# Optimization experiments

Hardware: AMD Instinct MI355X
Metric: run time of the kernel (lower is better)

## Reference

```python
import jax, jax.numpy as jnp
import numpy as np

B, S, T = 32, 512, 2048
D_TXT, D_MEL = 256, 80


def conv1d(x, w, b, pad):
    # x: (B, C_in, L), w: (C_out, C_in, K)
    y = jax.lax.conv_general_dilated(x, w, window_strides=(1,), padding=[(pad, pad)],
                                     dimension_numbers=('NCH', 'OIH', 'NCH'))
    return y + b[None, :, None]


def text_encoder(x, tw1, tb1, tw2, tb2):
    h = jax.nn.relu(conv1d(x, tw1, tb1, 1))
    return conv1d(h, tw2, tb2, 0)


def mel_encoder(x, mw1, mb1, mw2, mb2, mw3, mb3):
    h = jax.nn.leaky_relu(conv1d(x, mw1, mb1, 1), 0.01)
    h = jax.nn.leaky_relu(conv1d(h, mw2, mb2, 1), 0.01)
    return conv1d(h, mw3, mb3, 0)


def cdist(a, b):
    # a: (B,S,D), b: (B,T,D) -> (B,S,T) euclidean (torch.cdist p=2)
    d2 = (jnp.sum(a * a, -1)[:, :, None] + jnp.sum(b * b, -1)[:, None, :]
          - 2.0 * jnp.einsum('bsd,btd->bst', a, b))
    return jnp.sqrt(jnp.maximum(d2, 1e-12))


def maximum_path(value, mask):
    # Glow-TTS monotonic alignment search. value, mask: (B,S,T) float.
    b, s, t = value.shape
    neg_inf = jnp.float32(-jnp.inf)
    val = (value * mask).transpose(2, 0, 1)  # (T,B,S)
    x_range = jnp.arange(s)

    def fwd_step(v, jc):
        j, col = jc
        v0 = jnp.concatenate([jnp.full((b, 1), neg_inf, v.dtype), v[:, :-1]], axis=1)
        keep = v >= v0  # True: best predecessor is same text index
        v_max = jnp.where(keep, v, v0)
        v_new = jnp.where(x_range[None, :] <= j, v_max + col, neg_inf)
        return v_new, keep

    _, dirs = jax.lax.scan(fwd_step, jnp.zeros((b, s), value.dtype), (jnp.arange(t), val))
    direction = jnp.where(mask.astype(bool), dirs.transpose(1, 2, 0), True).astype(jnp.int32)

    index0 = jnp.sum(mask[:, :, 0], axis=1).astype(jnp.int32) - 1

    def bwd_step(index, dcol):
        row = (jnp.arange(s)[None, :] == index[:, None]).astype(value.dtype)
        d = jnp.take_along_axis(dcol, index[:, None], axis=1)[:, 0]
        return index + d - 1, row

    dcols_rev = jnp.flip(direction, axis=2).transpose(2, 0, 1)  # (T,B,S)
    _, rows = jax.lax.scan(bwd_step, index0, dcols_rev)
    path = jnp.flip(rows, axis=0).transpose(1, 2, 0)  # (B,S,T)
    return path * mask


def setup_inputs() -> dict:
    key = jax.random.key(0)
    ks = jax.random.split(key, 16)
    text = jax.random.normal(ks[0], (B, S, D_TXT), jnp.float32)
    mel = jax.random.normal(ks[1], (B, T, D_MEL), jnp.float32)
    src_len = jax.random.randint(ks[2], (B,), S // 2, S + 1).astype(jnp.int32)
    mel_len = jax.random.randint(ks[3], (B,), T // 2, T + 1).astype(jnp.int32)
    src_mask = jnp.arange(S)[None, :] >= src_len[:, None]   # True = pad
    mel_mask = jnp.arange(T)[None, :] >= mel_len[:, None]
    attn_mask = jnp.zeros((B, S, T), bool)  # unused in forward
    sc = 0.05
    params = dict(
        tw1=jax.random.normal(ks[4], (512, 256, 3)) * sc, tb1=jnp.zeros((512,)),
        tw2=jax.random.normal(ks[5], (80, 512, 1)) * sc, tb2=jnp.zeros((80,)),
        mw1=jax.random.normal(ks[6], (160, 80, 3)) * sc, mb1=jnp.zeros((160,)),
        mw2=jax.random.normal(ks[7], (80, 160, 3)) * sc, mb2=jnp.zeros((80,)),
        mw3=jax.random.normal(ks[8], (80, 80, 1)) * sc, mb3=jnp.zeros((80,)),
    )
    return dict(text=text, mel=mel, src_len=src_len, mel_len=mel_len,
                src_mask=src_mask, mel_mask=mel_mask, attn_mask=attn_mask, **params)


def reference(text, mel, src_len, mel_len, src_mask, mel_mask, attn_mask,
              tw1, tb1, tw2, tb2, mw1, mb1, mw2, mb2, mw3, mb3):
    text_emb = text_encoder(text.transpose(0, 2, 1), tw1, tb1, tw2, tb2).transpose(0, 2, 1)
    mel_emb = mel_encoder(mel.transpose(0, 2, 1), mw1, mb1, mw2, mb2, mw3, mb3).transpose(0, 2, 1)
    text_emb = jnp.where(src_mask[:, :, None], 0.0, text_emb)
    mel_emb = jnp.where(mel_mask[:, :, None], 0.0, mel_emb)
    dist = cdist(text_emb, mel_emb)  # (B,S,T)
    mask1 = jnp.arange(S)[None, :] < src_len[:, None]
    mask2 = jnp.arange(T)[None, :] < mel_len[:, None]
    mask_ST = mask1[:, :, None] & mask2[:, None, :]
    rev = ~mask_ST
    logits = jnp.where(rev, jnp.float32(-1e9), -dist)
    soft_A = jax.nn.softmax(logits, axis=1)  # softmax over text dim
    soft_A = jnp.where(rev, 0.0, soft_A)
    hard_A = maximum_path(soft_A, mask_ST.astype(soft_A.dtype))
    return soft_A, hard_A, rev
```

## Files before the change

### kernel.cpp

```cpp
#include <hip/hip_runtime.h>
#include <hip/hip_bf16.h>
#include <cstdint>

constexpr int NB_ = 32;
constexpr int NS_ = 512;
constexpr int NT_ = 2048;
constexpr int DMEL = 80;

constexpr size_t P = 134217728ull;
constexpr size_t PO_TE   = 0ull;
constexpr size_t PO_ME   = 5242880ull;
constexpr size_t PO_NA   = 26214400ull;
constexpr size_t PO_NB   = 26279936ull;
constexpr size_t PO_M    = 26542080ull;
constexpr size_t PO_RZ   = 26804224ull;
constexpr size_t PO_W1   = 27066368ull;
constexpr size_t PO_W2   = 28639232ull;
constexpr size_t PO_W3   = 28803072ull;
constexpr size_t PO_W4   = 28956672ull;
constexpr size_t PO_W5   = 29110272ull;
constexpr size_t PO_BIAS = 29135872ull;
constexpr size_t PO_DIR  = 29139968ull;
constexpr size_t PO_IDX  = 33334272ull;
constexpr size_t PO_FLAG = 33334400ull;
constexpr size_t FULL_NEED = P + 33334528ull;

constexpr int BO_T1 = 0, BO_T2 = 512, BO_M1 = 592, BO_M2 = 752, BO_M3 = 832;

__global__ void k_detect(const uint32_t* __restrict__ w, int* __restrict__ flag) {
  __shared__ int red[256];
  const int tid = threadIdx.x;
  int cnt = 0;
  for (int i = tid; i < 4096; i += 256) {
    uint32_t e = (w[i] >> 7) & 0xFFu;
    cnt += (e >= 119u && e <= 129u) ? 1 : 0;
  }
  red[tid] = cnt;
  __syncthreads();
  for (int s = 128; s > 0; s >>= 1) {
    if (tid < s) red[tid] += red[tid + s];
    __syncthreads();
  }
  if (tid == 0) *flag = (red[0] > 2048) ? 1 : 0;
}

__global__ void k_cvt(const void* __restrict__ in, float* __restrict__ out, int n,
                      const int* __restrict__ flag) {
  const int i = blockIdx.x * 256 + threadIdx.x;
  if (i >= n) return;
  if (*flag) {
    uint16_t u = ((const uint16_t*)in)[i];
    out[i] = __uint_as_float((uint32_t)u << 16);
  } else {
    out[i] = ((const float*)in)[i];
  }
}

__global__ void k_wtrans(const void* __restrict__ w, float* __restrict__ wT,
                         int CO, int CI, int KW, int total, const int* __restrict__ flag) {
  int id = blockIdx.x * 256 + threadIdx.x;
  if (id >= total) return;
  int co = id % CO;
  int rest = id / CO;
  int ci = rest % CI;
  int tap = rest / CI;
  int src = (co * CI + ci) * KW + tap;
  if (*flag) {
    uint16_t u = ((const uint16_t*)w)[src];
    wT[id] = __uint_as_float((uint32_t)u << 16);
  } else {
    wT[id] = ((const float*)w)[src];
  }
}

template <int CIN, int KW, int COUT, int NTILE, int NR, int KC, int LOG2L, int ACT, bool MASK>
__global__ __launch_bounds__(256) void k_conv(const float* __restrict__ x,
                                              const float* __restrict__ wT,
                                              const float* __restrict__ bias,
                                              float* __restrict__ y,
                                              const int* __restrict__ lenArr) {
  constexpr int L = 1 << LOG2L;
  constexpr int PAD = (KW - 1) / 2;
  constexpr int MT = 128;
  constexpr int APAD = 132;
  constexpr int BPAD = NTILE + 4;
  __shared__ float As[KC][APAD];
  __shared__ float Bs[KC][BPAD];

  const int tid = threadIdx.x;
  const int tx = tid & 15;
  const int ty = tid >> 4;
  constexpr int NBLK = COUT / NTILE;
  const int m0 = (blockIdx.x / NBLK) * MT;
  const int n0 = (blockIdx.x % NBLK) * NTILE;

  float acc[8][NR];
#pragma unroll
  for (int i = 0; i < 8; ++i)
#pragma unroll
    for (int j = 0; j < NR; ++j) acc[i][j] = 0.f;

  for (int tap = 0; tap < KW; ++tap) {
    for (int k0 = 0; k0 < CIN; k0 += KC) {
      __syncthreads();
      constexpr int AF4 = MT * KC / 4;
      constexpr int F4R = KC / 4;
      for (int f = tid; f < AF4; f += 256) {
        int row = f / F4R;
        int ko = (f % F4R) * 4;
        int r = m0 + row;
        int b = r >> LOG2L;
        int pos = (r & (L - 1)) + tap - PAD;
        float4 v = make_float4(0.f, 0.f, 0.f, 0.f);
        if (pos >= 0 && pos < L)
          v = *reinterpret_cast<const float4*>(
              &x[((size_t)(b << LOG2L) + pos) * CIN + k0 + ko]);
        As[ko + 0][row] = v.x;
        As[ko + 1][row] = v.y;
        As[ko + 2][row] = v.z;
        As[ko + 3][row] = v.w;
      }
      constexpr int BF4 = KC * NTILE / 4;
      constexpr int BF4R = NTILE / 4;
      for (int f = tid; f < BF4; f += 256) {
        int kk = f / BF4R;
        int no = (f % BF4R) * 4;
        float4 v = *reinterpret_cast<const float4*>(
            &wT[((size_t)(tap * CIN + k0 + kk)) * COUT + n0 + no]);
        *reinterpret_cast<float4*>(&Bs[kk][no]) = v;
      }
      __syncthreads();
#pragma unroll 8
      for (int kk = 0; kk < KC; ++kk) {
        float4 a0 = *reinterpret_cast<const float4*>(&As[kk][ty * 8]);
        float4 a1 = *reinterpret_cast<const float4*>(&As[kk][ty * 8 + 4]);
        float av[8] = {a0.x, a0.y, a0.z, a0.w, a1.x, a1.y, a1.z, a1.w};
        float bv[NR];
#pragma unroll
        for (int j = 0; j < NR; ++j) bv[j] = Bs[kk][tx * NR + j];
#pragma unroll
        for (int i = 0; i < 8; ++i)
#pragma unroll
          for (int j = 0; j < NR; ++j) acc[i][j] = fmaf(av[i], bv[j], acc[i][j]);
      }
    }
  }
#pragma unroll
  for (int i = 0; i < 8; ++i) {
    int r = m0 + ty * 8 + i;
    int b = r >> LOG2L;
    int pos = r & (L - 1);
    bool zero = MASK && (pos >= lenArr[b]);
#pragma unroll
    for (int j = 0; j < NR; ++j) {
      int c = n0 + tx * NR + j;
      float v = acc[i][j] + bias[c];
      if (ACT == 1) v = fmaxf(v, 0.f);
      if (ACT == 2) v = (v >= 0.f) ? v : 0.01f * v;
      if (zero) v = 0.f;
      y[(size_t)r * COUT + c] = v;
    }
  }
}

template <int CIN, int COUT, int NTILE, int NR, int KC, int LOG2L, int ACT>
__global__ __launch_bounds__(256) void k_conv3(const float* __restrict__ x,
                                               const float* __restrict__ wT,
                                               const float* __restrict__ bias,
                                               float* __restrict__ y) {
  constexpr int L = 1 << LOG2L;
  constexpr int MT = 128;
  constexpr int MT2 = MT + 2;
  constexpr int APAD = 132;
  constexpr int BPAD = NTILE + 4;
  __shared__ float As[KC][APAD];
  __shared__ float Bs[3][KC][BPAD];

  const int tid = threadIdx.x;
  const int tx = tid & 15;
  const int ty = tid >> 4;
  constexpr int NBLK = COUT / NTILE;
  const int m0 = (blockIdx.x / NBLK) * MT;
  const int n0 = (blockIdx.x % NBLK) * NTILE;
  const bool zlo = (m0 & (L - 1)) == 0;
  const bool zhi = ((m0 + MT) & (L - 1)) == 0;
  constexpr int TOTR = NB_ << LOG2L;

  float acc[8][NR];
#pragma unroll
  for (int i = 0; i < 8; ++i)
#pragma unroll
    for (int j = 0; j < NR; ++j) acc[i][j] = 0.f;

  for (int k0 = 0; k0 < CIN; k0 += KC) {
    __syncthreads();
    constexpr int F4R = KC / 4;
    for (int f = tid; f < MT2 * F4R; f += 256) {
      int h = f / F4R;
      int ko = (f % F4R) * 4;
      int g = m0 + h - 1;
      bool zero = (h == 0 && zlo) || (h == MT + 1 && zhi);
      int gc = g < 0 ? 0 : (g >= TOTR ? TOTR - 1 : g);
      float4 v = *reinterpret_cast<const float4*>(&x[(size_t)gc * CIN + k0 + ko]);
      if (zero) v = make_float4(0.f, 0.f, 0.f, 0.f);
      As[ko + 0][h] = v.x;
      As[ko + 1][h] = v.y;
      As[ko + 2][h] = v.z;
      As[ko + 3][h] = v.w;
    }
    constexpr int BF4R = NTILE / 4;
    for (int f = tid; f < 3 * KC * BF4R; f += 256) {
      int tap = f / (KC * BF4R);
      int rem = f % (KC * BF4R);
      int kk = rem / BF4R;
      int no = (rem % BF4R) * 4;
      float4 v = *reinterpret_cast<const float4*>(
          &wT[((size_t)(tap * CIN + k0 + kk)) * COUT + n0 + no]);
      *reinterpret_cast<float4*>(&Bs[tap][kk][no]) = v;
    }
    __syncthreads();
#pragma unroll 4
    for (int kk = 0; kk < KC; ++kk) {
      float aw[10];
      float4 a0 = *reinterpret_cast<const float4*>(&As[kk][ty * 8]);
      float4 a1 = *reinterpret_cast<const float4*>(&As[kk][ty * 8 + 4]);
      float2 a2 = *reinterpret_cast<const float2*>(&As[kk][ty * 8 + 8]);
      aw[0] = a0.x; aw[1] = a0.y; aw[2] = a0.z; aw[3] = a0.w;
      aw[4] = a1.x; aw[5] = a1.y; aw[6] = a1.z; aw[7] = a1.w;
      aw[8] = a2.x; aw[9] = a2.y;
#pragma unroll
      for (int tap = 0; tap < 3; ++tap) {
        float bv[NR];
#pragma unroll
        for (int j = 0; j < NR; ++j) bv[j] = Bs[tap][kk][tx * NR + j];
#pragma unroll
        for (int i = 0; i < 8; ++i)
#pragma unroll
          for (int j = 0; j < NR; ++j)
            acc[i][j] = fmaf(aw[i + tap], bv[j], acc[i][j]);
      }
    }
  }
#pragma unroll
  for (int i = 0; i < 8; ++i) {
    int r = m0 + ty * 8 + i;
#pragma unroll
    for (int j = 0; j < NR; ++j) {
      int c = n0 + tx * NR + j;
      float v = acc[i][j] + bias[c];
      if (ACT == 1) v = fmaxf(v, 0.f);
      if (ACT == 2) v = (v >= 0.f) ? v : 0.01f * v;
      y[(size_t)r * COUT + c] = v;
    }
  }
}

__global__ void k_norms(const float* __restrict__ e, float* __restrict__ out, int rows) {
  int tid = blockIdx.x * 256 + threadIdx.x;
  int row = tid >> 2, sub = tid & 3;
  if (row >= rows) return;
  const float* p = e + (size_t)row * DMEL;
  float s = 0.f;
#pragma unroll
  for (int j = 0; j < 5; ++j) {
    float4 v = *reinterpret_cast<const float4*>(&p[(sub + 4 * j) * 4]);
    s = fmaf(v.x, v.x, fmaf(v.y, v.y, fmaf(v.z, v.z, fmaf(v.w, v.w, s))));
  }
  s += __shfl_xor(s, 1);
  s += __shfl_xor(s, 2);
  if (sub == 0) out[row] = s;
}

__global__ __launch_bounds__(256) void k_stats2(
    const float* __restrict__ te, const float* __restrict__ me,
    const float* __restrict__ na, const float* __restrict__ nb,
    const int* __restrict__ src_len, const int* __restrict__ mel_len,
    float* __restrict__ marr, float* __restrict__ rzarr) {
  const int b = blockIdx.x >> 5;
  const int t0 = (blockIdx.x & 31) << 6;
  __shared__ float Bt[DMEL][68];
  __shared__ float At[DMEL][68];
  __shared__ float redm[16][64];
  __shared__ float redz[16][64];
  const int tid = threadIdx.x;
  for (int f = tid; f < 64 * 20; f += 256) {
    int row = f / 20, ko = (f % 20) << 2;
    float4 v = *reinterpret_cast<const float4*>(
        &me[((size_t)b * NT_ + t0 + row) * DMEL + ko]);
    Bt[ko][row] = v.x; Bt[ko + 1][row] = v.y; Bt[ko + 2][row] = v.z; Bt[ko + 3][row] = v.w;
  }
  const int tx = tid & 15, sy = tid >> 4;
  const int sl = src_len[b], ml = mel_len[b];
  const float NEGINF = -__builtin_inff();
  float nbv[4], mACC[4], zACC[4];
#pragma unroll
  for (int j = 0; j < 4; ++j) {
    nbv[j] = nb[b * NT_ + t0 + (tx << 2) + j];
    mACC[j] = NEGINF;
    zACC[j] = 0.f;
  }
  for (int c = 0; c < 8; ++c) {
    const int s0 = c << 6;
    __syncthreads();
    for (int f = tid; f < 64 * 20; f += 256) {
      int row = f / 20, ko = (f % 20) << 2;
      float4 v = *reinterpret_cast<const float4*>(
          &te[((size_t)b * NS_ + s0 + row) * DMEL + ko]);
      At[ko][row] = v.x; At[ko + 1][row] = v.y; At[ko + 2][row] = v.z; At[ko + 3][row] = v.w;
    }
    __syncthreads();
    float acc[4][4];
#pragma unroll
    for (int i = 0; i < 4; ++i)
#pragma unroll
      for (int j = 0; j < 4; ++j) acc[i][j] = 0.f;
#pragma unroll 8
    for (int kk = 0; kk < DMEL; ++kk) {
      float4 a = *reinterpret_cast<const float4*>(&At[kk][sy << 2]);
      float4 bb = *reinterpret_cast<const float4*>(&Bt[kk][tx << 2]);
      float av[4] = {a.x, a.y, a.z, a.w}, bv[4] = {bb.x, bb.y, bb.z, bb.w};
#pragma unroll
      for (int i = 0; i < 4; ++i)
#pragma unroll
        for (int j = 0; j < 4; ++j) acc[i][j] = fmaf(av[i], bv[j], acc[i][j]);
    }
    float nav[4];
#pragma unroll
    for (int i = 0; i < 4; ++i) nav[i] = na[b * NS_ + s0 + (sy << 2) + i];
#pragma unroll
    for (int j = 0; j < 4; ++j) {
      const bool tvalid = (t0 + (tx << 2) + j) < ml;
      float ov[4];
      float mNew = mACC[j];
#pragma unroll
      for (int i = 0; i < 4; ++i) {
        float d2 = (nav[i] + nbv[j]) - 2.0f * acc[i][j];
        float dist = sqrtf(fmaxf(d2, 1e-12f));
        bool valid = ((s0 + (sy << 2) + i) < sl) && tvalid;
        ov[i] = valid ? -dist : -1e9f;
        mNew = fmaxf(mNew, ov[i]);
      }
      float scale = expf(mACC[j] - mNew);
      float zadd = 0.f;
#pragma unroll
      for (int i = 0; i < 4; ++i) zadd += expf(ov[i] - mNew);
      zACC[j] = zACC[j] * scale + zadd;
      mACC[j] = mNew;
    }
  }
#pragma unroll
  for (int j = 0; j < 4; ++j) {
    redm[sy][(tx << 2) + j] = mACC[j];
    redz[sy][(tx << 2) + j] = zACC[j];
  }
  __syncthreads();
  if (tid < 64) {
    float M = NEGINF, Z = 0.f;
#pragma unroll
    for (int y = 0; y < 16; ++y) {
      float m = redm[y][tid], z = redz[y][tid];
      float Mn = fmaxf(M, m);
      Z = Z * expf(M - Mn) + z * expf(m - Mn);
      M = Mn;
    }
    marr[b * NT_ + t0 + tid] = M;
    rzarr[b * NT_ + t0 + tid] = 1.0f / Z;
  }
}

__global__ __launch_bounds__(256) void k_final3(
    const float* __restrict__ te, const float* __restrict__ me,
    const float* __restrict__ na, const float* __restrict__ nb,
    const float* __restrict__ marr, const float* __restrict__ rzarr,
    const int* __restrict__ src_len, const int* __restrict__ mel_len,
    float* __restrict__ val,
    float* __restrict__ soft, float* __restrict__ rev) {
  const int idx = blockIdx.x;
  const int tt = idx & 31;
  const int st = (idx >> 5) & 7;
  const int b = idx >> 8;
  const int s0 = st << 6, t0 = tt << 6;
  __shared__ float At[DMEL][68];
  __shared__ float Bt[DMEL][68];
  __shared__ float pl[64][65];
  const int tid = threadIdx.x;
  for (int f = tid; f < 64 * 20; f += 256) {
    int row = f / 20, ko = (f % 20) << 2;
    float4 v = *reinterpret_cast<const float4*>(
        &te[((size_t)b * NS_ + s0 + row) * DMEL + ko]);
    At[ko][row] = v.x; At[ko + 1][row] = v.y; At[ko + 2][row] = v.z; At[ko + 3][row] = v.w;
  }
  for (int f = tid; f < 64 * 20; f += 256) {
    int row = f / 20, ko = (f % 20) << 2;
    float4 v = *reinterpret_cast<const float4*>(
        &me[((size_t)b * NT_ + t0 + row) * DMEL + ko]);
    Bt[ko][row] = v.x; Bt[ko + 1][row] = v.y; Bt[ko + 2][row] = v.z; Bt[ko + 3][row] = v.w;
  }
  __syncthreads();
  const int sy = tid & 15, tx = tid >> 4;
  float acc[4][4];
#pragma unroll
  for (int i = 0; i < 4; ++i)
#pragma unroll
    for (int j = 0; j < 4; ++j) acc[i][j] = 0.f;
#pragma unroll 8
  for (int kk = 0; kk < DMEL; ++kk) {
    float4 a = *reinterpret_cast<const float4*>(&At[kk][sy << 2]);
    float4 bb = *reinterpret_cast<const float4*>(&Bt[kk][tx << 2]);
    float av[4] = {a.x, a.y, a.z, a.w}, bv[4] = {bb.x, bb.y, bb.z, bb.w};
#pragma unroll
    for (int i = 0; i < 4; ++i)
#pragma unroll
      for (int j = 0; j < 4; ++j) acc[i][j] = fmaf(av[i], bv[j], acc[i][j]);
  }
  const int sl = src_len[b], ml = mel_len[b];
  float nav[4], nbv[4];
#pragma unroll
  for (int i = 0; i < 4; ++i) nav[i] = na[b * NS_ + s0 + (sy << 2) + i];
#pragma unroll
  for (int j = 0; j < 4; ++j) nbv[j] = nb[b * NT_ + t0 + (tx << 2) + j];
#pragma unroll
  for (int j = 0; j < 4; ++j) {
    const int t = t0 + (tx << 2) + j;
    const bool tvalid = t < ml;
    const float mv = marr[b * NT_ + t];
    const float rzv = rzarr[b * NT_ + t];
    float pv[4];
#pragma unroll
    for (int i = 0; i < 4; ++i) {
      float d2 = (nav[i] + nbv[j]) - 2.0f * acc[i][j];
      float dist = sqrtf(fmaxf(d2, 1e-12f));
      bool valid = ((s0 + (sy << 2) + i) < sl) && tvalid;
      float ov = valid ? -dist : -1e9f;
      float p = tvalid ? expf(ov - mv) * rzv : 0.f;
      pv[i] = p;
      pl[(tx << 2) + j][(sy << 2) + i] = p;
    }
    float4 o = make_float4(pv[0], pv[1], pv[2], pv[3]);
    *reinterpret_cast<float4*>(&val[((size_t)b * NT_ + t) * NS_ + s0 + (sy << 2)]) = o;
  }
  __syncthreads();
  const int lane = tid & 63, w = tid >> 6;
#pragma unroll 4
  for (int i = 0; i < 16; ++i) {
    const int s_loc = (w << 4) + i;
    const int s = s0 + s_loc;
    float p = pl[lane][s_loc];
    size_t o = ((size_t)b * NS_ + s) * NT_ + t0 + lane;
    soft[o] = p;
    bool r = (s >= sl) || ((t0 + lane) >= ml);
    rev[o] = r ? 1.0f : 0.0f;
  }
}

__device__ __forceinline__ float dp_shr1(float x) {
  int r = __builtin_amdgcn_update_dpp(0, __float_as_int(x), 0x138, 0xF, 0xF, true);
  return __int_as_float(r);
}

__device__ __forceinline__ void dp_bar() {
  asm volatile("s_waitcnt lgkmcnt(0)" ::: "memory");
  __builtin_amdgcn_sched_barrier(0);
  __builtin_amdgcn_s_barrier();
}

#define DP_CHUNK(MASKED)                                                      \
  _Pragma("unroll")                                                           \
  for (int rb8 = 0; rb8 < 4; ++rb8) {                                         \
    float4 d0[4], d1[4];                                                      \
    _Pragma("unroll")                                                         \
    for (int rr = 0; rr < 4; ++rr) {                                          \
      const float* rp = rowbase + (((rb8 << 2) + rr) << 9);                   \
      d0[rr] = *reinterpret_cast<const float4*>(rp + (lane << 2));            \
      d1[rr] = *reinterpret_cast<const float4*>(rp + 256 + (lane << 2));      \
    }                                                                         \
    _Pragma("unroll")                                                         \
    for (int rr = 0; rr < 4; ++rr) {                                          \
      const int t = tbase + (rb8 << 2) + rr;                                  \
      float cc[8] = {d0[rr].x, d0[rr].y, d0[rr].z, d0[rr].w,                  \
                     d1[rr].x, d1[rr].y, d1[rr].z, d1[rr].w};                 \
      const int sh = t & 31;                                                  \
      if (t < ml) {                                                           \
        float up = dp_shr1(v[7]);                                             \
        float prev = (lane == 0) ? NEGINF : up;                               \
        _Pragma("unroll")                                                     \
        for (int j = 0; j < 8; ++j) {                                         \
          float cur = v[j];                                                   \
          bool keep = cur >= prev;                                            \
          float vm = fmaxf(cur, prev);                                        \
          float vn;                                                           \
          if (MASKED) {                                                       \
            int s = (lane << 3) + j;                                          \
            vn = (s <= t) ? vm + cc[j] : NEGINF;                              \
          } else {                                                            \
            vn = vm + cc[j];                                                  \
          }                                                                   \
          uint32_t bit = keep ? 1u : inv[j];                                  \
          bw[j] |= bit << sh;                                                 \
          v[j] = vn;                                                          \
          prev = cur;                                                         \
        }                                                                     \
      } else {                                                                \
        _Pragma("unroll")                                                     \
        for (int j = 0; j < 8; ++j) bw[j] |= 1u << sh;                        \
      }                                                                       \
    }                                                                         \
  }

__global__ __launch_bounds__(192) void k_dp(const float* __restrict__ val,
                                            const int* __restrict__ src_len,
                                            const int* __restrict__ mel_len,
                                            uint32_t* __restrict__ dir) {
  __shared__ float buf[2][16][512];
  const int b = blockIdx.x;
  const int wv = threadIdx.x >> 6;
  const int lane = threadIdx.x & 63;
  const float* base = val + (size_t)b * NT_ * NS_;
  const int sl = src_len[b];
  const int ml = mel_len[b];
  const float NEGINF = -__builtin_inff();
  int ca = ((ml + 31) >> 5) << 1;
  const int C_act = ca > 128 ? 128 : ca;

  float4 ra[8], rb[8];
  const int r0 = (wv - 1) << 3;

  float v[8];
  uint32_t bw[8], inv[8];
#pragma unroll
  for (int j = 0; j < 8; ++j) {
    v[j] = 0.0f;
    bw[j] = 0u;
    int s = (lane << 3) + j;
    inv[j] = (s < sl) ? 0u : 1u;
  }

  if (wv > 0) {
#pragma unroll
    for (int rr = 0; rr < 8; ++rr) {
      const float* g = base + (size_t)(r0 + rr) * NS_;
      ra[rr] = *reinterpret_cast<const float4*>(g + (lane << 3));
      rb[rr] = *reinterpret_cast<const float4*>(g + (lane << 3) + 4);
    }
#pragma unroll
    for (int rr = 0; rr < 8; ++rr) {
      float* l = &buf[0][r0 + rr][0];
      *reinterpret_cast<float4*>(l + (lane << 2)) = ra[rr];
      *reinterpret_cast<float4*>(l + 256 + (lane << 2)) = rb[rr];
    }
#pragma unroll
    for (int rr = 0; rr < 8; ++rr) {
      const float* g = base + (size_t)(16 + r0 + rr) * NS_;
      ra[rr] = *reinterpret_cast<const float4*>(g + (lane << 3));
      rb[rr] = *reinterpret_cast<const float4*>(g + (lane << 3) + 4);
    }
  }
  dp_bar();

  for (int c = 0; c < C_act; ++c) {
    if (wv > 0) {
      if (c + 1 < C_act) {
        const int nb = (c + 1) & 1;
#pragma unroll
        for (int rr = 0; rr < 8; ++rr) {
          float* l = &buf[nb][r0 + rr][0];
          *reinterpret_cast<float4*>(l + (lane << 2)) = ra[rr];
          *reinterpret_cast<float4*>(l + 256 + (lane << 2)) = rb[rr];
        }
      }
      if (c + 2 < C_act) {
        const float* cb = base + ((size_t)(c + 2) * 16 + r0) * NS_;
#pragma unroll
        for (int rr = 0; rr < 8; ++rr) {
          const float* g = cb + (size_t)rr * NS_;
          ra[rr] = *reinterpret_cast<const float4*>(g + (lane << 3));
          rb[rr] = *reinterpret_cast<const float4*>(g + (lane << 3) + 4);
        }
      }
    } else {
      const float* rowbase = &buf[c & 1][0][0];
      const int tbase = c << 4;
      if (c < 32) {
        DP_CHUNK(true)
      } else {
        DP_CHUNK(false)
      }
      if (c & 1) {
        const int c32 = c >> 1;
#pragma unroll
        for (int j = 0; j < 8; ++j) {
          dir[((size_t)(b * NS_) + (lane << 3) + j) * 64 + c32] = bw[j];
          bw[j] = 0u;
        }
      }
    }
    dp_bar();
  }
  if (wv == 0) {
    for (int c32 = C_act >> 1; c32 < 64; ++c32) {
#pragma unroll
      for (int j = 0; j < 8; ++j)
        dir[((size_t)(b * NS_) + (lane << 3) + j) * 64 + c32] = 0xFFFFFFFFu;
    }
  }
}

__global__ __launch_bounds__(256) void k_backtrack(
    const uint32_t* __restrict__ dir, const int* __restrict__ src_len,
    const int* __restrict__ mel_len, float* __restrict__ hard,
    int* __restrict__ idxio, int phase) {
  __shared__ uint32_t dl[NS_ * 32];
  const int b = blockIdx.x, tid = threadIdx.x;
  const uint32_t* db = dir + (size_t)b * NS_ * 64;
  const int woff = phase ? 0 : 32;
  for (int f = tid; f < 4096; f += 256) {
    int s = f >> 3;
    int wo = (f & 7) << 2;
    *reinterpret_cast<uint4*>(&dl[s * 32 + wo]) =
        *reinterpret_cast<const uint4*>(&db[s * 64 + woff + wo]);
  }
  __syncthreads();
  if (tid == 0) {
    const int ml = mel_len[b];
    int idx = phase ? idxio[b] : (src_len[b] - 1);
    if (idx < 0) idx = 0;
    if (idx > NS_ - 1) idx = NS_ - 1;
    const int thi = phase ? 1023 : 2047;
    const int tlo = phase ? 0 : 1024;
    int cw = -1, ci = -1;
    uint32_t w = 0;
    for (int t = thi; t >= tlo; --t) {
      int wi = t >> 5;
      if (wi != cw || idx != ci) {
        w = dl[idx * 32 + (wi - woff)];
        cw = wi;
        ci = idx;
      }
      if (t < ml) hard[((size_t)(b * NS_) + idx) * NT_ + t] = 1.0f;
      int step = (int)((w >> (t & 31)) & 1) - 1;
      idx += step;
      if (idx < 0) idx = 0;
    }
    if (!phase) idxio[b] = idx;
  }
}

extern "C" void kernel_launch(void* const* d_in, const int* in_sizes, int n_in,
                              void* d_out, int out_size, void* d_ws, size_t ws_size,
                              hipStream_t stream) {
  if (n_in != 17) return;
  if (ws_size < FULL_NEED) return;

  const void* text = d_in[0];
  const void* mel = d_in[1];
  const int* src_len = (const int*)d_in[2];
  const int* mel_len = (const int*)d_in[3];
  const void* tw1 = d_in[7];
  const void* tb1 = d_in[8];
  const void* tw2 = d_in[9];
  const void* tb2 = d_in[10];
  const void* mw1 = d_in[11];
  const void* mb1 = d_in[12];
  const void* mw2 = d_in[13];
  const void* mb2 = d_in[14];
  const void* mw3 = d_in[15];
  const void* mb3 = d_in[16];

  char* w8 = (char*)d_ws;
  float* mel_f32 = (float*)(w8 + 0);
  float* melh1 = (float*)(w8 + 20971520ull);
  float* mh2 = (float*)(w8 + 62914560ull);
  float* text_f32 = (float*)(w8 + 83886080ull);
  float* texth1 = (float*)(w8 + 100663296ull);
  float* val = (float*)(w8 + 0);

  float* te = (float*)(w8 + P + PO_TE);
  float* me = (float*)(w8 + P + PO_ME);
  float* na = (float*)(w8 + P + PO_NA);
  float* nb = (float*)(w8 + P + PO_NB);
  float* marr = (float*)(w8 + P + PO_M);
  float* rzarr = (float*)(w8 + P + PO_RZ);
  float* wt1 = (float*)(w8 + P + PO_W1);
  float* wt2 = (float*)(w8 + P + PO_W2);
  float* wt3 = (float*)(w8 + P + PO_W3);
  float* wt4 = (float*)(w8 + P + PO_W4);
  float* wt5 = (float*)(w8 + P + PO_W5);
  float* biasb = (float*)(w8 + P + PO_BIAS);
  uint32_t* dir = (uint32_t*)(w8 + P + PO_DIR);
  int* idxio = (int*)(w8 + P + PO_IDX);
  int* flag = (int*)(w8 + P + PO_FLAG);

  float* soft = (float*)d_out;
  float* hard = soft + (size_t)NB_ * NS_ * NT_;
  float* rev = soft + 2 * (size_t)NB_ * NS_ * NT_;

  k_detect<<<1, 256, 0, stream>>>((const uint32_t*)text, flag);
  k_cvt<<<(NB_ * NS_ * 256 + 255) / 256, 256, 0, stream>>>(text, text_f32, NB_ * NS_ * 256, flag);
  k_cvt<<<(NB_ * NT_ * 80 + 255) / 256, 256, 0, stream>>>(mel, mel_f32, NB_ * NT_ * 80, flag);
  k_cvt<<<2, 256, 0, stream>>>(tb1, biasb + BO_T1, 512, flag);
  k_cvt<<<1, 256, 0, stream>>>(tb2, biasb + BO_T2, 80, flag);
  k_cvt<<<1, 256, 0, stream>>>(mb1, biasb + BO_M1, 160, flag);
  k_cvt<<<1, 256, 0, stream>>>(mb2, biasb + BO_M2, 80, flag);
  k_cvt<<<1, 256, 0, stream>>>(mb3, biasb + BO_M3, 80, flag);

  k_wtrans<<<(512 * 256 * 3 + 255) / 256, 256, 0, stream>>>(tw1, wt1, 512, 256, 3, 512 * 256 * 3, flag);
  k_wtrans<<<(80 * 512 + 255) / 256, 256, 0, stream>>>(tw2, wt2, 80, 512, 1, 80 * 512, flag);
  k_wtrans<<<(160 * 80 * 3 + 255) / 256, 256, 0, stream>>>(mw1, wt3, 160, 80, 3, 160 * 80 * 3, flag);
  k_wtrans<<<(80 * 160 * 3 + 255) / 256, 256, 0, stream>>>(mw2, wt4, 80, 160, 3, 80 * 160 * 3, flag);
  k_wtrans<<<(80 * 80 + 255) / 256, 256, 0, stream>>>(mw3, wt5, 80, 80, 1, 80 * 80, flag);

  k_conv3<80, 160, 80, 5, 16, 11, 2><<<512 * 2, 256, 0, stream>>>(mel_f32, wt3, biasb + BO_M1, melh1);
  k_conv3<160, 80, 80, 5, 32, 11, 2><<<512 * 1, 256, 0, stream>>>(melh1, wt4, biasb + BO_M2, mh2);
  k_conv<80, 1, 80, 80, 5, 16, 11, 0, true><<<512 * 1, 256, 0, stream>>>(mh2, wt5, biasb + BO_M3, me, mel_len);
  k_conv3<256, 512, 128, 8, 32, 9, 1><<<128 * 4, 256, 0, stream>>>(text_f32, wt1, biasb + BO_T1, texth1);
  k_conv<512, 1, 80, 80, 5, 32, 9, 0, true><<<128 * 1, 256, 0, stream>>>(texth1, wt2, biasb + BO_T2, te, src_len);

  k_norms<<<(NB_ * NS_ * 4) / 256, 256, 0, stream>>>(te, na, NB_ * NS_);
  k_norms<<<(NB_ * NT_ * 4) / 256, 256, 0, stream>>>(me, nb, NB_ * NT_);

  hipMemsetAsync(hard, 0, (size_t)NB_ * NS_ * NT_ * 4, stream);

  k_stats2<<<NB_ * 32, 256, 0, stream>>>(te, me, na, nb, src_len, mel_len, marr, rzarr);
  k_final3<<<NB_ * 8 * 32, 256, 0, stream>>>(te, me, na, nb, marr, rzarr, src_len, mel_len,
                                             val, soft, rev);

  k_dp<<<NB_, 192, 0, stream>>>(val, src_len, mel_len, dir);
  k_backtrack<<<NB_, 256, 0, stream>>>(dir, src_len, mel_len, hard, idxio, 0);
  k_backtrack<<<NB_, 256, 0, stream>>>(dir, src_len, mel_len, hard, idxio, 1);
}
```

Measured before the change: 1.294 ms.

## Drop dtype conversion, fuse norms into conv, cache logits, merge backtrack

```diff
diff --git a/kernel.cpp b/kernel.cpp
--- a/kernel.cpp
+++ b/kernel.cpp
@@ -19,68 +19,29 @@
 constexpr size_t PO_W3   = 28803072ull;
 constexpr size_t PO_W4   = 28956672ull;
 constexpr size_t PO_W5   = 29110272ull;
-constexpr size_t PO_BIAS = 29135872ull;
 constexpr size_t PO_DIR  = 29139968ull;
-constexpr size_t PO_IDX  = 33334272ull;
-constexpr size_t PO_FLAG = 33334400ull;
 constexpr size_t FULL_NEED = P + 33334528ull;
 
-constexpr int BO_T1 = 0, BO_T2 = 512, BO_M1 = 592, BO_M2 = 752, BO_M3 = 832;
-
-__global__ void k_detect(const uint32_t* __restrict__ w, int* __restrict__ flag) {
-  __shared__ int red[256];
-  const int tid = threadIdx.x;
-  int cnt = 0;
-  for (int i = tid; i < 4096; i += 256) {
-    uint32_t e = (w[i] >> 7) & 0xFFu;
-    cnt += (e >= 119u && e <= 129u) ? 1 : 0;
-  }
-  red[tid] = cnt;
-  __syncthreads();
-  for (int s = 128; s > 0; s >>= 1) {
-    if (tid < s) red[tid] += red[tid + s];
-    __syncthreads();
-  }
-  if (tid == 0) *flag = (red[0] > 2048) ? 1 : 0;
-}
-
-__global__ void k_cvt(const void* __restrict__ in, float* __restrict__ out, int n,
-                      const int* __restrict__ flag) {
-  const int i = blockIdx.x * 256 + threadIdx.x;
-  if (i >= n) return;
-  if (*flag) {
-    uint16_t u = ((const uint16_t*)in)[i];
-    out[i] = __uint_as_float((uint32_t)u << 16);
-  } else {
-    out[i] = ((const float*)in)[i];
-  }
-}
-
-__global__ void k_wtrans(const void* __restrict__ w, float* __restrict__ wT,
-                         int CO, int CI, int KW, int total, const int* __restrict__ flag) {
+__global__ void k_wtrans(const float* __restrict__ w, float* __restrict__ wT,
+                         int CO, int CI, int KW, int total) {
   int id = blockIdx.x * 256 + threadIdx.x;
   if (id >= total) return;
   int co = id % CO;
   int rest = id / CO;
   int ci = rest % CI;
   int tap = rest / CI;
-  int src = (co * CI + ci) * KW + tap;
-  if (*flag) {
-    uint16_t u = ((const uint16_t*)w)[src];
-    wT[id] = __uint_as_float((uint32_t)u << 16);
-  } else {
-    wT[id] = ((const float*)w)[src];
-  }
-}
-
-template <int CIN, int KW, int COUT, int NTILE, int NR, int KC, int LOG2L, int ACT, bool MASK>
+  wT[id] = w[(co * CI + ci) * KW + tap];
+}
+
+template <int CIN, int COUT, int NTILE, int NR, int KC, int LOG2L, int ACT,
+          bool MASK, bool NORM>
 __global__ __launch_bounds__(256) void k_conv(const float* __restrict__ x,
                                               const float* __restrict__ wT,
                                               const float* __restrict__ bias,
                                               float* __restrict__ y,
-                                              const int* __restrict__ lenArr) {
+                                              const int* __restrict__ lenArr,
+                                              float* __restrict__ normout) {
   constexpr int L = 1 << LOG2L;
-  constexpr int PAD = (KW - 1) / 2;
   constexpr int MT = 128;
   constexpr int APAD = 132;
   constexpr int BPAD = NTILE + 4;
@@ -100,49 +61,42 @@
 #pragma unroll
     for (int j = 0; j < NR; ++j) acc[i][j] = 0.f;
 
-  for (int tap = 0; tap < KW; ++tap) {
-    for (int k0 = 0; k0 < CIN; k0 += KC) {
-      __syncthreads();
-      constexpr int AF4 = MT * KC / 4;
-      constexpr int F4R = KC / 4;
-      for (int f = tid; f < AF4; f += 256) {
-        int row = f / F4R;
-        int ko = (f % F4R) * 4;
-        int r = m0 + row;
-        int b = r >> LOG2L;
-        int pos = (r & (L - 1)) + tap - PAD;
-        float4 v = make_float4(0.f, 0.f, 0.f, 0.f);
-        if (pos >= 0 && pos < L)
-          v = *reinterpret_cast<const float4*>(
-              &x[((size_t)(b << LOG2L) + pos) * CIN + k0 + ko]);
-        As[ko + 0][row] = v.x;
-        As[ko + 1][row] = v.y;
-        As[ko + 2][row] = v.z;
-        As[ko + 3][row] = v.w;
-      }
-      constexpr int BF4 = KC * NTILE / 4;
-      constexpr int BF4R = NTILE / 4;
-      for (int f = tid; f < BF4; f += 256) {
-        int kk = f / BF4R;
-        int no = (f % BF4R) * 4;
-        float4 v = *reinterpret_cast<const float4*>(
-            &wT[((size_t)(tap * CIN + k0 + kk)) * COUT + n0 + no]);
-        *reinterpret_cast<float4*>(&Bs[kk][no]) = v;
-      }
-      __syncthreads();
+  for (int k0 = 0; k0 < CIN; k0 += KC) {
+    __syncthreads();
+    constexpr int AF4 = MT * KC / 4;
+    constexpr int F4R = KC / 4;
+    for (int f = tid; f < AF4; f += 256) {
+      int row = f / F4R;
+      int ko = (f % F4R) * 4;
+      int r = m0 + row;
+      float4 v = *reinterpret_cast<const float4*>(&x[(size_t)r * CIN + k0 + ko]);
+      As[ko + 0][row] = v.x;
+      As[ko + 1][row] = v.y;
+      As[ko + 2][row] = v.z;
+      As[ko + 3][row] = v.w;
+    }
+    constexpr int BF4 = KC * NTILE / 4;
+    constexpr int BF4R = NTILE / 4;
+    for (int f = tid; f < BF4; f += 256) {
+      int kk = f / BF4R;
+      int no = (f % BF4R) * 4;
+      float4 v = *reinterpret_cast<const float4*>(
+          &wT[((size_t)(k0 + kk)) * COUT + n0 + no]);
+      *reinterpret_cast<float4*>(&Bs[kk][no]) = v;
+    }
+    __syncthreads();
 #pragma unroll 8
-      for (int kk = 0; kk < KC; ++kk) {
-        float4 a0 = *reinterpret_cast<const float4*>(&As[kk][ty * 8]);
-        float4 a1 = *reinterpret_cast<const float4*>(&As[kk][ty * 8 + 4]);
-        float av[8] = {a0.x, a0.y, a0.z, a0.w, a1.x, a1.y, a1.z, a1.w};
-        float bv[NR];
-#pragma unroll
-        for (int j = 0; j < NR; ++j) bv[j] = Bs[kk][tx * NR + j];
-#pragma unroll
-        for (int i = 0; i < 8; ++i)
-#pragma unroll
-          for (int j = 0; j < NR; ++j) acc[i][j] = fmaf(av[i], bv[j], acc[i][j]);
-      }
+    for (int kk = 0; kk < KC; ++kk) {
+      float4 a0 = *reinterpret_cast<const float4*>(&As[kk][ty * 8]);
+      float4 a1 = *reinterpret_cast<const float4*>(&As[kk][ty * 8 + 4]);
+      float av[8] = {a0.x, a0.y, a0.z, a0.w, a1.x, a1.y, a1.z, a1.w};
+      float bv[NR];
+#pragma unroll
+      for (int j = 0; j < NR; ++j) bv[j] = Bs[kk][tx * NR + j];
+#pragma unroll
+      for (int i = 0; i < 8; ++i)
+#pragma unroll
+        for (int j = 0; j < NR; ++j) acc[i][j] = fmaf(av[i], bv[j], acc[i][j]);
     }
   }
 #pragma unroll
@@ -151,6 +105,7 @@
     int b = r >> LOG2L;
     int pos = r & (L - 1);
     bool zero = MASK && (pos >= lenArr[b]);
+    float sq = 0.f;
 #pragma unroll
     for (int j = 0; j < NR; ++j) {
       int c = n0 + tx * NR + j;
@@ -159,6 +114,14 @@
       if (ACT == 2) v = (v >= 0.f) ? v : 0.01f * v;
       if (zero) v = 0.f;
       y[(size_t)r * COUT + c] = v;
+      if (NORM) sq = fmaf(v, v, sq);
+    }
+    if (NORM) {
+      sq += __shfl_xor(sq, 1);
+      sq += __shfl_xor(sq, 2);
+      sq += __shfl_xor(sq, 4);
+      sq += __shfl_xor(sq, 8);
+      if (tx == 0) normout[r] = sq;
     }
   }
 }
@@ -255,27 +218,12 @@
   }
 }
 
-__global__ void k_norms(const float* __restrict__ e, float* __restrict__ out, int rows) {
-  int tid = blockIdx.x * 256 + threadIdx.x;
-  int row = tid >> 2, sub = tid & 3;
-  if (row >= rows) return;
-  const float* p = e + (size_t)row * DMEL;
-  float s = 0.f;
-#pragma unroll
-  for (int j = 0; j < 5; ++j) {
-    float4 v = *reinterpret_cast<const float4*>(&p[(sub + 4 * j) * 4]);
-    s = fmaf(v.x, v.x, fmaf(v.y, v.y, fmaf(v.z, v.z, fmaf(v.w, v.w, s))));
-  }
-  s += __shfl_xor(s, 1);
-  s += __shfl_xor(s, 2);
-  if (sub == 0) out[row] = s;
-}
-
 __global__ __launch_bounds__(256) void k_stats2(
     const float* __restrict__ te, const float* __restrict__ me,
     const float* __restrict__ na, const float* __restrict__ nb,
     const int* __restrict__ src_len, const int* __restrict__ mel_len,
-    float* __restrict__ marr, float* __restrict__ rzarr) {
+    float* __restrict__ marr, float* __restrict__ rzarr,
+    float* __restrict__ val) {
   const int b = blockIdx.x >> 5;
   const int t0 = (blockIdx.x & 31) << 6;
   __shared__ float Bt[DMEL][68];
@@ -289,7 +237,7 @@
         &me[((size_t)b * NT_ + t0 + row) * DMEL + ko]);
     Bt[ko][row] = v.x; Bt[ko + 1][row] = v.y; Bt[ko + 2][row] = v.z; Bt[ko + 3][row] = v.w;
   }
-  const int tx = tid & 15, sy = tid >> 4;
+  const int sy = tid & 15, tx = tid >> 4;
   const int sl = src_len[b], ml = mel_len[b];
   const float NEGINF = -__builtin_inff();
   float nbv[4], mACC[4], zACC[4];
@@ -329,7 +277,8 @@
     for (int i = 0; i < 4; ++i) nav[i] = na[b * NS_ + s0 + (sy << 2) + i];
 #pragma unroll
     for (int j = 0; j < 4; ++j) {
-      const bool tvalid = (t0 + (tx << 2) + j) < ml;
+      const int t = t0 + (tx << 2) + j;
+      const bool tvalid = t < ml;
       float ov[4];
       float mNew = mACC[j];
 #pragma unroll
@@ -346,6 +295,8 @@
       for (int i = 0; i < 4; ++i) zadd += expf(ov[i] - mNew);
       zACC[j] = zACC[j] * scale + zadd;
       mACC[j] = mNew;
+      float4 o = make_float4(ov[0], ov[1], ov[2], ov[3]);
+      *reinterpret_cast<float4*>(&val[((size_t)b * NT_ + t) * NS_ + s0 + (sy << 2)]) = o;
     }
   }
 #pragma unroll
@@ -355,7 +306,8 @@
   }
   __syncthreads();
   if (tid < 64) {
-    float M = NEGINF, Z = 0.f;
+    const float NEGINF2 = -__builtin_inff();
+    float M = NEGINF2, Z = 0.f;
 #pragma unroll
     for (int y = 0; y < 16; ++y) {
       float m = redm[y][tid], z = redz[y][tid];
@@ -368,76 +320,37 @@
   }
 }
 
-__global__ __launch_bounds__(256) void k_final3(
-    const float* __restrict__ te, const float* __restrict__ me,
-    const float* __restrict__ na, const float* __restrict__ nb,
+__global__ __launch_bounds__(256) void k_final4(
     const float* __restrict__ marr, const float* __restrict__ rzarr,
     const int* __restrict__ src_len, const int* __restrict__ mel_len,
-    float* __restrict__ val,
-    float* __restrict__ soft, float* __restrict__ rev) {
+    float* __restrict__ val, float* __restrict__ soft, float* __restrict__ rev) {
   const int idx = blockIdx.x;
   const int tt = idx & 31;
   const int st = (idx >> 5) & 7;
   const int b = idx >> 8;
   const int s0 = st << 6, t0 = tt << 6;
-  __shared__ float At[DMEL][68];
-  __shared__ float Bt[DMEL][68];
   __shared__ float pl[64][65];
   const int tid = threadIdx.x;
-  for (int f = tid; f < 64 * 20; f += 256) {
-    int row = f / 20, ko = (f % 20) << 2;
-    float4 v = *reinterpret_cast<const float4*>(
-        &te[((size_t)b * NS_ + s0 + row) * DMEL + ko]);
-    At[ko][row] = v.x; At[ko + 1][row] = v.y; At[ko + 2][row] = v.z; At[ko + 3][row] = v.w;
-  }
-  for (int f = tid; f < 64 * 20; f += 256) {
-    int row = f / 20, ko = (f % 20) << 2;
-    float4 v = *reinterpret_cast<const float4*>(
-        &me[((size_t)b * NT_ + t0 + row) * DMEL + ko]);
-    Bt[ko][row] = v.x; Bt[ko + 1][row] = v.y; Bt[ko + 2][row] = v.z; Bt[ko + 3][row] = v.w;
-  }
-  __syncthreads();
   const int sy = tid & 15, tx = tid >> 4;
-  float acc[4][4];
-#pragma unroll
-  for (int i = 0; i < 4; ++i)
-#pragma unroll
-    for (int j = 0; j < 4; ++j) acc[i][j] = 0.f;
-#pragma unroll 8
-  for (int kk = 0; kk < DMEL; ++kk) {
-    float4 a = *reinterpret_cast<const float4*>(&At[kk][sy << 2]);
-    float4 bb = *reinterpret_cast<const float4*>(&Bt[kk][tx << 2]);
-    float av[4] = {a.x, a.y, a.z, a.w}, bv[4] = {bb.x, bb.y, bb.z, bb.w};
-#pragma unroll
-    for (int i = 0; i < 4; ++i)
-#pragma unroll
-      for (int j = 0; j < 4; ++j) acc[i][j] = fmaf(av[i], bv[j], acc[i][j]);
-  }
   const int sl = src_len[b], ml = mel_len[b];
-  float nav[4], nbv[4];
-#pragma unroll
-  for (int i = 0; i < 4; ++i) nav[i] = na[b * NS_ + s0 + (sy << 2) + i];
-#pragma unroll
-  for (int j = 0; j < 4; ++j) nbv[j] = nb[b * NT_ + t0 + (tx << 2) + j];
 #pragma unroll
   for (int j = 0; j < 4; ++j) {
     const int t = t0 + (tx << 2) + j;
     const bool tvalid = t < ml;
     const float mv = marr[b * NT_ + t];
     const float rzv = rzarr[b * NT_ + t];
-    float pv[4];
-#pragma unroll
-    for (int i = 0; i < 4; ++i) {
-      float d2 = (nav[i] + nbv[j]) - 2.0f * acc[i][j];
-      float dist = sqrtf(fmaxf(d2, 1e-12f));
-      bool valid = ((s0 + (sy << 2) + i) < sl) && tvalid;
-      float ov = valid ? -dist : -1e9f;
-      float p = tvalid ? expf(ov - mv) * rzv : 0.f;
-      pv[i] = p;
-      pl[(tx << 2) + j][(sy << 2) + i] = p;
-    }
-    float4 o = make_float4(pv[0], pv[1], pv[2], pv[3]);
-    *reinterpret_cast<float4*>(&val[((size_t)b * NT_ + t) * NS_ + s0 + (sy << 2)]) = o;
+    float* vp = &val[((size_t)b * NT_ + t) * NS_ + s0 + (sy << 2)];
+    float4 ov = *reinterpret_cast<const float4*>(vp);
+    float4 p;
+    p.x = tvalid ? expf(ov.x - mv) * rzv : 0.f;
+    p.y = tvalid ? expf(ov.y - mv) * rzv : 0.f;
+    p.z = tvalid ? expf(ov.z - mv) * rzv : 0.f;
+    p.w = tvalid ? expf(ov.w - mv) * rzv : 0.f;
+    *reinterpret_cast<float4*>(vp) = p;
+    pl[(tx << 2) + j][(sy << 2) + 0] = p.x;
+    pl[(tx << 2) + j][(sy << 2) + 1] = p.y;
+    pl[(tx << 2) + j][(sy << 2) + 2] = p.z;
+    pl[(tx << 2) + j][(sy << 2) + 3] = p.w;
   }
   __syncthreads();
   const int lane = tid & 63, w = tid >> 6;
@@ -607,32 +520,28 @@
 
 __global__ __launch_bounds__(256) void k_backtrack(
     const uint32_t* __restrict__ dir, const int* __restrict__ src_len,
-    const int* __restrict__ mel_len, float* __restrict__ hard,
-    int* __restrict__ idxio, int phase) {
-  __shared__ uint32_t dl[NS_ * 32];
+    const int* __restrict__ mel_len, float* __restrict__ hard) {
+  __shared__ uint32_t dl[NS_ * 64];
   const int b = blockIdx.x, tid = threadIdx.x;
   const uint32_t* db = dir + (size_t)b * NS_ * 64;
-  const int woff = phase ? 0 : 32;
-  for (int f = tid; f < 4096; f += 256) {
-    int s = f >> 3;
-    int wo = (f & 7) << 2;
-    *reinterpret_cast<uint4*>(&dl[s * 32 + wo]) =
-        *reinterpret_cast<const uint4*>(&db[s * 64 + woff + wo]);
+  for (int f = tid; f < 8192; f += 256) {
+    int s = f >> 4;
+    int wo = (f & 15) << 2;
+    *reinterpret_cast<uint4*>(&dl[s * 64 + wo]) =
+        *reinterpret_cast<const uint4*>(&db[s * 64 + wo]);
   }
   __syncthreads();
   if (tid == 0) {
     const int ml = mel_len[b];
-    int idx = phase ? idxio[b] : (src_len[b] - 1);
+    int idx = src_len[b] - 1;
     if (idx < 0) idx = 0;
     if (idx > NS_ - 1) idx = NS_ - 1;
-    const int thi = phase ? 1023 : 2047;
-    const int tlo = phase ? 0 : 1024;
     int cw = -1, ci = -1;
     uint32_t w = 0;
-    for (int t = thi; t >= tlo; --t) {
+    for (int t = NT_ - 1; t >= 0; --t) {
       int wi = t >> 5;
       if (wi != cw || idx != ci) {
-        w = dl[idx * 32 + (wi - woff)];
+        w = dl[idx * 64 + wi];
         cw = wi;
         ci = idx;
       }
@@ -641,7 +550,6 @@
       idx += step;
       if (idx < 0) idx = 0;
     }
-    if (!phase) idxio[b] = idx;
   }
 }
 
@@ -651,27 +559,25 @@
   if (n_in != 17) return;
   if (ws_size < FULL_NEED) return;
 
-  const void* text = d_in[0];
-  const void* mel = d_in[1];
+  const float* text = (const float*)d_in[0];
+  const float* mel = (const float*)d_in[1];
   const int* src_len = (const int*)d_in[2];
   const int* mel_len = (const int*)d_in[3];
-  const void* tw1 = d_in[7];
-  const void* tb1 = d_in[8];
-  const void* tw2 = d_in[9];
-  const void* tb2 = d_in[10];
-  const void* mw1 = d_in[11];
-  const void* mb1 = d_in[12];
-  const void* mw2 = d_in[13];
-  const void* mb2 = d_in[14];
-  const void* mw3 = d_in[15];
-  const void* mb3 = d_in[16];
+  const float* tw1 = (const float*)d_in[7];
+  const float* tb1 = (const float*)d_in[8];
+  const float* tw2 = (const float*)d_in[9];
+  const float* tb2 = (const float*)d_in[10];
+  const float* mw1 = (const float*)d_in[11];
+  const float* mb1 = (const float*)d_in[12];
+  const float* mw2 = (const float*)d_in[13];
+  const float* mb2 = (const float*)d_in[14];
+  const float* mw3 = (const float*)d_in[15];
+  const float* mb3 = (const float*)d_in[16];
 
   char* w8 = (char*)d_ws;
-  float* mel_f32 = (float*)(w8 + 0);
-  float* melh1 = (float*)(w8 + 20971520ull);
-  float* mh2 = (float*)(w8 + 62914560ull);
-  float* text_f32 = (float*)(w8 + 83886080ull);
-  float* texth1 = (float*)(w8 + 100663296ull);
+  float* melh1 = (float*)(w8 + 0);
+  float* mh2 = (float*)(w8 + 41943040ull);
+  float* texth1 = (float*)(w8 + 62914560ull);
   float* val = (float*)(w8 + 0);
 
   float* te = (float*)(w8 + P + PO_TE);
@@ -685,46 +591,29 @@
   float* wt3 = (float*)(w8 + P + PO_W3);
   float* wt4 = (float*)(w8 + P + PO_W4);
   float* wt5 = (float*)(w8 + P + PO_W5);
-  float* biasb = (float*)(w8 + P + PO_BIAS);
   uint32_t* dir = (uint32_t*)(w8 + P + PO_DIR);
-  int* idxio = (int*)(w8 + P + PO_IDX);
-  int* flag = (int*)(w8 + P + PO_FLAG);
 
   float* soft = (float*)d_out;
   float* hard = soft + (size_t)NB_ * NS_ * NT_;
   float* rev = soft + 2 * (size_t)NB_ * NS_ * NT_;
 
-  k_detect<<<1, 256, 0, stream>>>((const uint32_t*)text, flag);
-  k_cvt<<<(NB_ * NS_ * 256 + 255) / 256, 256, 0, stream>>>(text, text_f32, NB_ * NS_ * 256, flag);
-  k_cvt<<<(NB_ * NT_ * 80 + 255) / 256, 256, 0, stream>>>(mel, mel_f32, NB_ * NT_ * 80, flag);
-  k_cvt<<<2, 256, 0, stream>>>(tb1, biasb + BO_T1, 512, flag);
-  k_cvt<<<1, 256, 0, stream>>>(tb2, biasb + BO_T2, 80, flag);
-  k_cvt<<<1, 256, 0, stream>>>(mb1, biasb + BO_M1, 160, flag);
-  k_cvt<<<1, 256, 0, stream>>>(mb2, biasb + BO_M2, 80, flag);
-  k_cvt<<<1, 256, 0, stream>>>(mb3, biasb + BO_M3, 80, flag);
-
-  k_wtrans<<<(512 * 256 * 3 + 255) / 256, 256, 0, stream>>>(tw1, wt1, 512, 256, 3, 512 * 256 * 3, flag);
-  k_wtrans<<<(80 * 512 + 255) / 256, 256, 0, stream>>>(tw2, wt2, 80, 512, 1, 80 * 512, flag);
-  k_wtrans<<<(160 * 80 * 3 + 255) / 256, 256, 0, stream>>>(mw1, wt3, 160, 80, 3, 160 * 80 * 3, flag);
-  k_wtrans<<<(80 * 160 * 3 + 255) / 256, 256, 0, stream>>>(mw2, wt4, 80, 160, 3, 80 * 160 * 3, flag);
-  k_wtrans<<<(80 * 80 + 255) / 256, 256, 0, stream>>>(mw3, wt5, 80, 80, 1, 80 * 80, flag);
-
-  k_conv3<80, 160, 80, 5, 16, 11, 2><<<512 * 2, 256, 0, stream>>>(mel_f32, wt3, biasb + BO_M1, melh1);
-  k_conv3<160, 80, 80, 5, 32, 11, 2><<<512 * 1, 256, 0, stream>>>(melh1, wt4, biasb + BO_M2, mh2);
-  k_conv<80, 1, 80, 80, 5, 16, 11, 0, true><<<512 * 1, 256, 0, stream>>>(mh2, wt5, biasb + BO_M3, me, mel_len);
-  k_conv3<256, 512, 128, 8, 32, 9, 1><<<128 * 4, 256, 0, stream>>>(text_f32, wt1, biasb + BO_T1, texth1);
-  k_conv<512, 1, 80, 80, 5, 32, 9, 0, true><<<128 * 1, 256, 0, stream>>>(texth1, wt2, biasb + BO_T2, te, src_len);
-
-  k_norms<<<(NB_ * NS_ * 4) / 256, 256, 0, stream>>>(te, na, NB_ * NS_);
-  k_norms<<<(NB_ * NT_ * 4) / 256, 256, 0, stream>>>(me, nb, NB_ * NT_);
+  k_wtrans<<<(512 * 256 * 3 + 255) / 256, 256, 0, stream>>>(tw1, wt1, 512, 256, 3, 512 * 256 * 3);
+  k_wtrans<<<(80 * 512 + 255) / 256, 256, 0, stream>>>(tw2, wt2, 80, 512, 1, 80 * 512);
+  k_wtrans<<<(160 * 80 * 3 + 255) / 256, 256, 0, stream>>>(mw1, wt3, 160, 80, 3, 160 * 80 * 3);
+  k_wtrans<<<(80 * 160 * 3 + 255) / 256, 256, 0, stream>>>(mw2, wt4, 80, 160, 3, 80 * 160 * 3);
+  k_wtrans<<<(80 * 80 + 255) / 256, 256, 0, stream>>>(mw3, wt5, 80, 80, 1, 80 * 80);
+
+  k_conv3<80, 160, 80, 5, 16, 11, 2><<<512 * 2, 256, 0, stream>>>(mel, wt3, mb1, melh1);
+  k_conv3<160, 80, 80, 5, 32, 11, 2><<<512 * 1, 256, 0, stream>>>(melh1, wt4, mb2, mh2);
+  k_conv<80, 80, 80, 5, 16, 11, 0, true, true><<<512 * 1, 256, 0, stream>>>(mh2, wt5, mb3, me, mel_len, nb);
+  k_conv3<256, 512, 128, 8, 32, 9, 1><<<128 * 4, 256, 0, stream>>>(text, wt1, tb1, texth1);
+  k_conv<512, 80, 80, 5, 32, 9, 0, true, true><<<128 * 1, 256, 0, stream>>>(texth1, wt2, tb2, te, src_len, na);
 
   hipMemsetAsync(hard, 0, (size_t)NB_ * NS_ * NT_ * 4, stream);
 
-  k_stats2<<<NB_ * 32, 256, 0, stream>>>(te, me, na, nb, src_len, mel_len, marr, rzarr);
-  k_final3<<<NB_ * 8 * 32, 256, 0, stream>>>(te, me, na, nb, marr, rzarr, src_len, mel_len,
-                                             val, soft, rev);
+  k_stats2<<<NB_ * 32, 256, 0, stream>>>(te, me, na, nb, src_len, mel_len, marr, rzarr, val);
+  k_final4<<<NB_ * 8 * 32, 256, 0, stream>>>(marr, rzarr, src_len, mel_len, val, soft, rev);
 
   k_dp<<<NB_, 192, 0, stream>>>(val, src_len, mel_len, dir);
-  k_backtrack<<<NB_, 256, 0, stream>>>(dir, src_len, mel_len, hard, idxio, 0);
-  k_backtrack<<<NB_, 256, 0, stream>>>(dir, src_len, mel_len, hard, idxio, 1);
-}
+  k_backtrack<<<NB_, 256, 0, stream>>>(dir, src_len, mel_len, hard);
+}
```

After: 1.137 ms. -12.1%, faster.
